# Kernel optimization log

Hardware: AMD Instinct MI355X
Metric: run time of the kernel (lower is better)

Reference implementation:

```python
import jax, jax.numpy as jnp
import numpy as np

K_NEIGHBOURS = 16


def setup_inputs() -> dict:
    key = jax.random.key(0)
    k1, k2 = jax.random.split(key)
    receivers = jax.random.normal(k1, (8, 2048, 128), dtype=jnp.float32)
    senders = jax.random.normal(k2, (8, 2048, 128), dtype=jnp.float32)
    return {"receivers": receivers, "senders": senders}


def reference(receivers, senders):
    B, Ns, Fs = senders.shape
    Nr = receivers.shape[1]
    k = K_NEIGHBOURS

    # pairwise squared euclidean distances [B, Ns, Nr]
    mixed = -2.0 * jnp.einsum('bsf,brf->bsr', senders, receivers)
    x2 = jnp.sum(senders * senders, axis=-1)[:, :, None]
    y2 = jnp.sum(receivers * receivers, axis=-1)[:, None, :]
    dist = jnp.abs(mixed + x2 + y2)

    # k nearest receivers per sender (no self_connection handling: default False)
    _, idx = jax.lax.top_k(-dist, k)  # [B, Ns, k]
    # tf.boolean_mask flattens in row-major order, so edges appear in
    # ascending receiver-index order within each sender row
    idx = jnp.sort(idx, axis=-1)

    # dense sender connectivity matrix (== sum of one-hots over k)
    b_ix = jnp.arange(B)[:, None, None]
    s_ix = jnp.arange(Ns)[None, :, None]
    sender = jnp.zeros((B, Ns, Nr), dtype=senders.dtype).at[b_ix, s_ix, idx].set(1.0)

    # gather edge endpoints; connectivity entries are exactly 1 so the
    # sender-matrix multiply + boolean_mask reduces to a plain gather
    sending = jnp.broadcast_to(senders[:, :, None, :], (B, Ns, k, Fs)).reshape(B * Ns * k, Fs)
    receiving = receivers[b_ix, idx].reshape(B * Ns * k, receivers.shape[-1])  # [B,Ns,k,Fr]

    edges = jnp.concatenate([sending, receiving], axis=-1)  # 'concat' aggregation
    return edges, sender
```

## Files before the change

kernel.cpp:

```cpp
#include <hip/hip_runtime.h>
#include <cstdint>

#define K_NE 16
constexpr int B = 8, N = 2048, F = 128;
constexpr size_t NSEND = (size_t)B * N;
constexpr size_t EDGE_FLOATS = NSEND * K_NE * 256;
constexpr size_t SEND_FLOATS = (size_t)B * N * N;

typedef _Float16 half8 __attribute__((ext_vector_type(8)));
typedef _Float16 half2v __attribute__((ext_vector_type(2)));
typedef float floatx4 __attribute__((ext_vector_type(4)));

#define SCALE 2048.0f
#define INV_SC2 2.384185791015625e-07f
#define F16_MIN_NORM 6.103515625e-05f

__global__ __launch_bounds__(256) void prep_kernel(const float* __restrict__ S,
                                                   const float* __restrict__ Rv,
                                                   float* __restrict__ x2,
                                                   float* __restrict__ y2,
                                                   _Float16* __restrict__ SH,
                                                   _Float16* __restrict__ SL,
                                                   _Float16* __restrict__ RH,
                                                   _Float16* __restrict__ RL) {
    const int tid = blockIdx.x * 256 + threadIdx.x;
    const int w = tid >> 6, lane = tid & 63;
    const bool isR = w >= (int)NSEND;
    const int row = isR ? w - (int)NSEND : w;
    const float* X = isR ? Rv : S;
    _Float16* H = isR ? RH : SH;
    _Float16* L = isR ? RL : SL;
    float* nrm = isR ? y2 : x2;

    const float2 v = ((const float2*)(X + (size_t)row * F))[lane];
    float s = v.x * v.x + v.y * v.y;
    #pragma unroll
    for (int off = 32; off; off >>= 1) s += __shfl_xor(s, off);
    if (lane == 0) nrm[row] = s;

    const float a0 = v.x * SCALE, a1 = v.y * SCALE;
    _Float16 h0 = (_Float16)a0;
    if (fabsf((float)h0) < F16_MIN_NORM) h0 = (_Float16)0.0f;
    _Float16 l0 = (_Float16)(a0 - (float)h0);
    if (fabsf((float)l0) < F16_MIN_NORM) l0 = (_Float16)0.0f;
    _Float16 h1 = (_Float16)a1;
    if (fabsf((float)h1) < F16_MIN_NORM) h1 = (_Float16)0.0f;
    _Float16 l1 = (_Float16)(a1 - (float)h1);
    if (fabsf((float)l1) < F16_MIN_NORM) l1 = (_Float16)0.0f;
    half2v hv = {h0, h1}, lv = {l0, l1};
    *(half2v*)(H + (size_t)row * F + lane * 2) = hv;
    *(half2v*)(L + (size_t)row * F + lane * 2) = lv;
}

__global__ __launch_bounds__(512) void score_mfma_kernel(
        const _Float16* __restrict__ SH, const _Float16* __restrict__ SL,
        const _Float16* __restrict__ RH, const _Float16* __restrict__ RL,
        const float* __restrict__ x2, const float* __restrict__ y2,
        float* __restrict__ scores) {
    __shared__ __attribute__((aligned(16))) _Float16 lA[2][2][4][128][8];
    __shared__ __attribute__((aligned(16))) _Float16 lB[2][2][4][128][8];
    const int bx = blockIdx.x, by = blockIdx.y, bz = blockIdx.z;
    const int t = threadIdx.x, lane = t & 63, wv = t >> 6;
    const int wrow0 = (wv >> 2) * 64;
    const int wcol0 = (wv & 3) * 32;
    const int lr = lane & 15, kg = lane >> 4;

    int s_h[2], s_kg[2], s_row[2];
    #pragma unroll
    for (int i = 0; i < 2; ++i) {
        const int s = t + (i << 9);
        s_h[i]   = s >> 9;
        s_row[i] = (s & 511) >> 2;
        s_kg[i]  = s & 3;
    }
    const size_t baseA = (size_t)(bz * N + by * 128);
    const size_t baseB = (size_t)(bz * N + bx * 128);

    #pragma unroll
    for (int i = 0; i < 2; ++i) {
        const _Float16* sa = (s_h[i] ? SL : SH) + (baseA + s_row[i]) * F + s_kg[i] * 8;
        const _Float16* sb = (s_h[i] ? RL : RH) + (baseB + s_row[i]) * F + s_kg[i] * 8;
        *(half8*)&lA[0][s_h[i]][s_kg[i]][s_row[i]][0] = *(const half8*)sa;
        *(half8*)&lB[0][s_h[i]][s_kg[i]][s_row[i]][0] = *(const half8*)sb;
    }
    __syncthreads();

    floatx4 acc[4][2] = {};

    #pragma unroll
    for (int kc = 0; kc < 4; ++kc) {
        const int cur = kc & 1;
        half8 pa[2], pb[2];
        if (kc < 3) {
            const int ko = (kc + 1) * 32;
            #pragma unroll
            for (int i = 0; i < 2; ++i) {
                pa[i] = *(const half8*)((s_h[i] ? SL : SH) + (baseA + s_row[i]) * F + ko + s_kg[i] * 8);
                pb[i] = *(const half8*)((s_h[i] ? RL : RH) + (baseB + s_row[i]) * F + ko + s_kg[i] * 8);
            }
        }
        half8 ah[4], al[4];
        #pragma unroll
        for (int i = 0; i < 4; ++i) {
            ah[i] = *(const half8*)&lA[cur][0][kg][wrow0 + i * 16 + lr][0];
            al[i] = *(const half8*)&lA[cur][1][kg][wrow0 + i * 16 + lr][0];
        }
        #pragma unroll
        for (int j = 0; j < 2; ++j) {
            const half8 bh = *(const half8*)&lB[cur][0][kg][wcol0 + j * 16 + lr][0];
            const half8 bl = *(const half8*)&lB[cur][1][kg][wcol0 + j * 16 + lr][0];
            #pragma unroll
            for (int i = 0; i < 4; ++i) {
                acc[i][j] = __builtin_amdgcn_mfma_f32_16x16x32_f16(ah[i], bh, acc[i][j], 0, 0, 0);
                acc[i][j] = __builtin_amdgcn_mfma_f32_16x16x32_f16(ah[i], bl, acc[i][j], 0, 0, 0);
                acc[i][j] = __builtin_amdgcn_mfma_f32_16x16x32_f16(al[i], bh, acc[i][j], 0, 0, 0);
            }
        }
        if (kc < 3) {
            const int nxt = cur ^ 1;
            #pragma unroll
            for (int i = 0; i < 2; ++i) {
                *(half8*)&lA[nxt][s_h[i]][s_kg[i]][s_row[i]][0] = pa[i];
                *(half8*)&lB[nxt][s_h[i]][s_kg[i]][s_row[i]][0] = pb[i];
            }
            __syncthreads();
        }
    }

    float* outb = scores + (size_t)bz * N * N;
    const float* x2b = x2 + (size_t)bz * N;
    const float* y2b = y2 + (size_t)bz * N;
    #pragma unroll
    for (int j = 0; j < 2; ++j) {
        const int col = bx * 128 + wcol0 + j * 16 + lr;
        const float yv = y2b[col];
        #pragma unroll
        for (int i = 0; i < 4; ++i) {
            #pragma unroll
            for (int r = 0; r < 4; ++r) {
                const int row = by * 128 + wrow0 + i * 16 + (lane >> 4) * 4 + r;
                const float d = acc[i][j][r] * INV_SC2;
                outb[(size_t)row * N + col] = fabsf((-2.0f * d + x2b[row]) + yv);
            }
        }
    }
}

#define KEYC(U, C) ((C) == 0 ? (U).x : (C) == 1 ? (U).y : (C) == 2 ? (U).z : (U).w)

__global__ __launch_bounds__(256) void topk_fused_kernel(const float* __restrict__ S,
                                                         const float* __restrict__ Rv,
                                                         float* __restrict__ scores,
                                                         float* __restrict__ edges_out) {
    __shared__ double candbuf[4][64];
    const int t = threadIdx.x;
    const int lane = t & 63;
    const int w = t >> 6;
    const int g = blockIdx.x * 4 + w;
    const int bz = g >> 11;
    double* cbuf = candbuf[w];
    float* srowp = scores + (size_t)g * N;
    const uint4* sr = (const uint4*)srowp;
    const double MAGIC = 4503599627370496.0;

    uint4 u[8];
    uint32_t mk = 0xFFFFFFFFu;
    #pragma unroll
    for (int jj = 0; jj < 8; ++jj) {
        u[jj] = sr[jj * 64 + lane];
        mk = mk < u[jj].x ? mk : u[jj].x;
        mk = mk < u[jj].y ? mk : u[jj].y;
        mk = mk < u[jj].z ? mk : u[jj].z;
        mk = mk < u[jj].w ? mk : u[jj].w;
    }

    uint32_t v = mk;
    #pragma unroll
    for (int k = 2; k <= 64; k <<= 1) {
        #pragma unroll
        for (int j = k >> 1; j >= 1; j >>= 1) {
            uint32_t o = (uint32_t)__shfl_xor((int)v, j);
            const bool take_min = (((lane & j) == 0) == ((lane & k) == 0));
            const uint32_t mn = v < o ? v : o;
            const uint32_t mx = v < o ? o : v;
            v = take_min ? mn : mx;
        }
    }
    const uint32_t T16 = (uint32_t)__shfl((int)v, 15);

    int myc = 0;
    #pragma unroll
    for (int jj = 0; jj < 8; ++jj)
        #pragma unroll
        for (int c = 0; c < 4; ++c)
            myc += (KEYC(u[jj], c) <= T16) ? 1 : 0;
    int off = myc;
    #pragma unroll
    for (int d = 1; d < 64; d <<= 1) {
        const int o = __shfl_up(off, d);
        if (lane >= d) off += o;
    }
    const int total = __shfl(off, 63);
    const int base = off - myc;

    int ixs[16];
    if (total <= 64) {
        int p = base;
        #pragma unroll
        for (int jj = 0; jj < 8; ++jj)
            #pragma unroll
            for (int c = 0; c < 4; ++c) {
                const uint32_t key = KEYC(u[jj], c);
                if (key <= T16) {
                    cbuf[p] = (double)key * 2048.0 + (double)(jj * 256 + lane * 4 + c);
                    ++p;
                }
            }
        double d = (lane < total) ? cbuf[lane] : 1e300;
        #pragma unroll
        for (int k = 2; k <= 64; k <<= 1) {
            #pragma unroll
            for (int j = k >> 1; j >= 1; j >>= 1) {
                const double o = __shfl_xor(d, j);
                const bool take_min = (((lane & j) == 0) == ((lane & k) == 0));
                d = take_min ? fmin(d, o) : fmax(d, o);
            }
        }
        const int myidx = (int)(__double_as_longlong(d + MAGIC) & 2047);
        #pragma unroll
        for (int e = 0; e < 16; ++e) ixs[e] = __shfl(myidx, e);
    } else {
        uint32_t fk = 0xFFFFFFFFu, fi = 0;
        #pragma unroll
        for (int jj = 0; jj < 8; ++jj) {
            const uint32_t bse = (uint32_t)(jj * 256 + lane * 4);
            if (u[jj].x < fk) { fk = u[jj].x; fi = bse; }
            if (u[jj].y < fk) { fk = u[jj].y; fi = bse + 1; }
            if (u[jj].z < fk) { fk = u[jj].z; fi = bse + 2; }
            if (u[jj].w < fk) { fk = u[jj].w; fi = bse + 3; }
        }
        #pragma unroll
        for (int it = 0; it < 16; ++it) {
            const uint32_t ck = fk, ci = fi;
            uint32_t gk = fk, gi = fi;
            #pragma unroll
            for (int o2 = 32; o2; o2 >>= 1) {
                uint32_t ok = (uint32_t)__shfl_xor((int)gk, o2);
                uint32_t oi = (uint32_t)__shfl_xor((int)gi, o2);
                if (ok < gk || (ok == gk && oi < gi)) { gk = ok; gi = oi; }
            }
            ixs[it] = (int)gi;
            if (ck == gk && ci == gi) {
                const int djj = (int)(gi >> 8), dc = (int)(gi & 3);
                #pragma unroll
                for (int jj = 0; jj < 8; ++jj)
                    if (jj == djj) {
                        if (dc == 0) u[jj].x = 0xFFFFFFFFu;
                        else if (dc == 1) u[jj].y = 0xFFFFFFFFu;
                        else if (dc == 2) u[jj].z = 0xFFFFFFFFu;
                        else u[jj].w = 0xFFFFFFFFu;
                    }
                fk = 0xFFFFFFFFu; fi = 0;
                #pragma unroll
                for (int jj = 0; jj < 8; ++jj) {
                    const uint32_t bse = (uint32_t)(jj * 256 + lane * 4);
                    if (u[jj].x < fk) { fk = u[jj].x; fi = bse; }
                    if (u[jj].y < fk) { fk = u[jj].y; fi = bse + 1; }
                    if (u[jj].z < fk) { fk = u[jj].z; fi = bse + 2; }
                    if (u[jj].w < fk) { fk = u[jj].w; fi = bse + 3; }
                }
            }
        }
    }

    int rank[16];
    #pragma unroll
    for (int e = 0; e < 16; ++e) {
        int r = 0;
        #pragma unroll
        for (int f = 0; f < 16; ++f) r += (ixs[f] < ixs[e]) ? 1 : 0;
        rank[e] = r;
    }

    uint32_t mask = 0;
    #pragma unroll
    for (int e = 0; e < 16; ++e) {
        const int ix = ixs[e];
        const int lane_t = (ix >> 2) & 63;
        const int bitpos = ((ix >> 8) << 2) | (ix & 3);
        if (lane == lane_t) mask |= (1u << bitpos);
    }
    #pragma unroll
    for (int j = 0; j < 8; ++j) {
        float4 vv;
        vv.x = (mask >> (j * 4 + 0)) & 1u ? 1.f : 0.f;
        vv.y = (mask >> (j * 4 + 1)) & 1u ? 1.f : 0.f;
        vv.z = (mask >> (j * 4 + 2)) & 1u ? 1.f : 0.f;
        vv.w = (mask >> (j * 4 + 3)) & 1u ? 1.f : 0.f;
        *(float4*)(srowp + j * 256 + lane * 4) = vv;
    }

    const float* srow = S + (size_t)g * F;
    const float* rb = Rv + (size_t)bz * N * F;
    float4 vs = {0.f, 0.f, 0.f, 0.f};
    if (lane < 32) vs = *(const float4*)(srow + lane * 4);
    #pragma unroll
    for (int e = 0; e < 16; ++e) {
        float4 vv = vs;
        if (lane >= 32)
            vv = *(const float4*)(rb + (size_t)ixs[e] * F + (lane - 32) * 4);
        *(float4*)(edges_out + ((size_t)g * K_NE + rank[e]) * 256 + lane * 4) = vv;
    }
}

extern "C" void kernel_launch(void* const* d_in, const int* in_sizes, int n_in,
                              void* d_out, int out_size, void* d_ws, size_t ws_size,
                              hipStream_t stream) {
    (void)in_sizes; (void)n_in; (void)out_size; (void)ws_size;
    const float* recv = (const float*)d_in[0];
    const float* send = (const float*)d_in[1];
    float* out = (float*)d_out;
    float* sender_mat = out + EDGE_FLOATS;
    float* x2 = (float*)((char*)d_ws + (262144u * 4));
    float* y2 = x2 + NSEND;

    _Float16* SH = (_Float16*)out;
    _Float16* SL = SH + NSEND * F;
    _Float16* RH = SL + NSEND * F;
    _Float16* RL = RH + NSEND * F;

    prep_kernel<<<8192, 256, 0, stream>>>(send, recv, x2, y2, SH, SL, RH, RL);
    dim3 g1(16, 16, 8);
    score_mfma_kernel<<<g1, 512, 0, stream>>>(SH, SL, RH, RL, x2, y2, sender_mat);
    topk_fused_kernel<<<4096, 256, 0, stream>>>(send, recv, sender_mat, out);
}
```

Baseline: 157.1 us.

## Fuse score MFMA and top-k into one kernel with scores held in LDS

The separate f16 hi/lo prep, tiled score GEMM and top-k kernels are replaced by one fused kernel. Each 1024-thread block takes 16 senders, computes their distances to all 2048 receivers with MFMA, keeps them in a 128KB LDS buffer, and runs top-k from there. This removes the full B×N×N score write and read-back through global memory. In exchange every block re-reads and re-converts all receivers from fp32, so receiver data reuse drops to 16 rows per block, and the large LDS footprint allows only one block per CU.

```diff
diff --git a/kernel.cpp b/kernel.cpp
--- a/kernel.cpp
+++ b/kernel.cpp
@@ -5,169 +5,119 @@
 constexpr int B = 8, N = 2048, F = 128;
 constexpr size_t NSEND = (size_t)B * N;
 constexpr size_t EDGE_FLOATS = NSEND * K_NE * 256;
-constexpr size_t SEND_FLOATS = (size_t)B * N * N;
+constexpr int SPB = 16;
 
 typedef _Float16 half8 __attribute__((ext_vector_type(8)));
-typedef _Float16 half2v __attribute__((ext_vector_type(2)));
 typedef float floatx4 __attribute__((ext_vector_type(4)));
 
 #define SCALE 2048.0f
 #define INV_SC2 2.384185791015625e-07f
 #define F16_MIN_NORM 6.103515625e-05f
 
-__global__ __launch_bounds__(256) void prep_kernel(const float* __restrict__ S,
-                                                   const float* __restrict__ Rv,
-                                                   float* __restrict__ x2,
-                                                   float* __restrict__ y2,
-                                                   _Float16* __restrict__ SH,
-                                                   _Float16* __restrict__ SL,
-                                                   _Float16* __restrict__ RH,
-                                                   _Float16* __restrict__ RL) {
-    const int tid = blockIdx.x * 256 + threadIdx.x;
-    const int w = tid >> 6, lane = tid & 63;
-    const bool isR = w >= (int)NSEND;
-    const int row = isR ? w - (int)NSEND : w;
-    const float* X = isR ? Rv : S;
-    _Float16* H = isR ? RH : SH;
-    _Float16* L = isR ? RL : SL;
-    float* nrm = isR ? y2 : x2;
-
-    const float2 v = ((const float2*)(X + (size_t)row * F))[lane];
+__global__ __launch_bounds__(256) void norms_kernel(const float* __restrict__ X,
+                                                    float* __restrict__ out) {
+    int tid = blockIdx.x * 256 + threadIdx.x;
+    int w = tid >> 6, lane = tid & 63;
+    const float2 v = ((const float2*)(X + (size_t)w * F))[lane];
     float s = v.x * v.x + v.y * v.y;
     #pragma unroll
     for (int off = 32; off; off >>= 1) s += __shfl_xor(s, off);
-    if (lane == 0) nrm[row] = s;
-
-    const float a0 = v.x * SCALE, a1 = v.y * SCALE;
-    _Float16 h0 = (_Float16)a0;
-    if (fabsf((float)h0) < F16_MIN_NORM) h0 = (_Float16)0.0f;
-    _Float16 l0 = (_Float16)(a0 - (float)h0);
-    if (fabsf((float)l0) < F16_MIN_NORM) l0 = (_Float16)0.0f;
-    _Float16 h1 = (_Float16)a1;
-    if (fabsf((float)h1) < F16_MIN_NORM) h1 = (_Float16)0.0f;
-    _Float16 l1 = (_Float16)(a1 - (float)h1);
-    if (fabsf((float)l1) < F16_MIN_NORM) l1 = (_Float16)0.0f;
-    half2v hv = {h0, h1}, lv = {l0, l1};
-    *(half2v*)(H + (size_t)row * F + lane * 2) = hv;
-    *(half2v*)(L + (size_t)row * F + lane * 2) = lv;
-}
-
-__global__ __launch_bounds__(512) void score_mfma_kernel(
-        const _Float16* __restrict__ SH, const _Float16* __restrict__ SL,
-        const _Float16* __restrict__ RH, const _Float16* __restrict__ RL,
-        const float* __restrict__ x2, const float* __restrict__ y2,
-        float* __restrict__ scores) {
-    __shared__ __attribute__((aligned(16))) _Float16 lA[2][2][4][128][8];
-    __shared__ __attribute__((aligned(16))) _Float16 lB[2][2][4][128][8];
-    const int bx = blockIdx.x, by = blockIdx.y, bz = blockIdx.z;
+    if (lane == 0) out[w] = s;
+}
+
+__device__ __forceinline__ void cvt_hilo(float a, _Float16& h, _Float16& l) {
+    a *= SCALE;
+    h = (_Float16)a;
+    if (fabsf((float)h) < F16_MIN_NORM) h = (_Float16)0.0f;
+    l = (_Float16)(a - (float)h);
+    if (fabsf((float)l) < F16_MIN_NORM) l = (_Float16)0.0f;
+}
+
+#define KEYC(U, C) ((C) == 0 ? (U).x : (C) == 1 ? (U).y : (C) == 2 ? (U).z : (U).w)
+
+__global__ __launch_bounds__(1024) void fused_kernel(const float* __restrict__ S,
+                                                     const float* __restrict__ Rv,
+                                                     const float* __restrict__ x2,
+                                                     const float* __restrict__ y2,
+                                                     float* __restrict__ conn,
+                                                     float* __restrict__ edges_out) {
+    __shared__ uint32_t keys[SPB][N];
+    __shared__ double candbuf[16][64];
     const int t = threadIdx.x, lane = t & 63, wv = t >> 6;
-    const int wrow0 = (wv >> 2) * 64;
-    const int wcol0 = (wv & 3) * 32;
-    const int lr = lane & 15, kg = lane >> 4;
-
-    int s_h[2], s_kg[2], s_row[2];
-    #pragma unroll
-    for (int i = 0; i < 2; ++i) {
-        const int s = t + (i << 9);
-        s_h[i]   = s >> 9;
-        s_row[i] = (s & 511) >> 2;
-        s_kg[i]  = s & 3;
-    }
-    const size_t baseA = (size_t)(bz * N + by * 128);
-    const size_t baseB = (size_t)(bz * N + bx * 128);
-
-    #pragma unroll
-    for (int i = 0; i < 2; ++i) {
-        const _Float16* sa = (s_h[i] ? SL : SH) + (baseA + s_row[i]) * F + s_kg[i] * 8;
-        const _Float16* sb = (s_h[i] ? RL : RH) + (baseB + s_row[i]) * F + s_kg[i] * 8;
-        *(half8*)&lA[0][s_h[i]][s_kg[i]][s_row[i]][0] = *(const half8*)sa;
-        *(half8*)&lB[0][s_h[i]][s_kg[i]][s_row[i]][0] = *(const half8*)sb;
+    const int blk = blockIdx.x;
+    const int bz = blk >> 7;
+    const int sg0 = (blk & 127) * SPB;
+    const int lr = lane & 15, kgrp = lane >> 4;
+    const double MAGIC = 4503599627370496.0;
+
+    const float* x2b = x2 + bz * N;
+    const float* y2b = y2 + bz * N;
+    const float* rbase = Rv + (size_t)bz * N * F;
+
+    half8 ah[4], al[4];
+    {
+        const float* arow = S + ((size_t)(bz * N + sg0) + lr) * F;
+        #pragma unroll
+        for (int ks = 0; ks < 4; ++ks) {
+            const int k0 = ks * 32 + kgrp * 8;
+            const float4 f0 = *(const float4*)(arow + k0);
+            const float4 f1 = *(const float4*)(arow + k0 + 4);
+            const float av[8] = {f0.x, f0.y, f0.z, f0.w, f1.x, f1.y, f1.z, f1.w};
+            #pragma unroll
+            for (int j = 0; j < 8; ++j) {
+                _Float16 hh, ll;
+                cvt_hilo(av[j], hh, ll);
+                ah[ks][j] = hh;
+                al[ks][j] = ll;
+            }
+        }
+    }
+    float xr[4];
+    #pragma unroll
+    for (int r = 0; r < 4; ++r) xr[r] = x2b[sg0 + kgrp * 4 + r];
+
+    #pragma unroll 1
+    for (int ct = 0; ct < 8; ++ct) {
+        const int col0 = wv * 128 + ct * 16;
+        const float* brow = rbase + (size_t)(col0 + lr) * F;
+        floatx4 acc = {0.f, 0.f, 0.f, 0.f};
+        #pragma unroll
+        for (int ks = 0; ks < 4; ++ks) {
+            const int k0 = ks * 32 + kgrp * 8;
+            const float4 f0 = *(const float4*)(brow + k0);
+            const float4 f1 = *(const float4*)(brow + k0 + 4);
+            const float bv[8] = {f0.x, f0.y, f0.z, f0.w, f1.x, f1.y, f1.z, f1.w};
+            half8 bh, bl;
+            #pragma unroll
+            for (int j = 0; j < 8; ++j) {
+                _Float16 hh, ll;
+                cvt_hilo(bv[j], hh, ll);
+                bh[j] = hh;
+                bl[j] = ll;
+            }
+            acc = __builtin_amdgcn_mfma_f32_16x16x32_f16(ah[ks], bh, acc, 0, 0, 0);
+            acc = __builtin_amdgcn_mfma_f32_16x16x32_f16(ah[ks], bl, acc, 0, 0, 0);
+            acc = __builtin_amdgcn_mfma_f32_16x16x32_f16(al[ks], bh, acc, 0, 0, 0);
+        }
+        const float yv = y2b[col0 + lr];
+        #pragma unroll
+        for (int r = 0; r < 4; ++r) {
+            const float d = acc[r] * INV_SC2;
+            const float sc = fabsf((-2.0f * d + xr[r]) + yv);
+            keys[kgrp * 4 + r][col0 + lr] = __float_as_uint(sc);
+        }
     }
     __syncthreads();
 
-    floatx4 acc[4][2] = {};
-
-    #pragma unroll
-    for (int kc = 0; kc < 4; ++kc) {
-        const int cur = kc & 1;
-        half8 pa[2], pb[2];
-        if (kc < 3) {
-            const int ko = (kc + 1) * 32;
-            #pragma unroll
-            for (int i = 0; i < 2; ++i) {
-                pa[i] = *(const half8*)((s_h[i] ? SL : SH) + (baseA + s_row[i]) * F + ko + s_kg[i] * 8);
-                pb[i] = *(const half8*)((s_h[i] ? RL : RH) + (baseB + s_row[i]) * F + ko + s_kg[i] * 8);
-            }
-        }
-        half8 ah[4], al[4];
-        #pragma unroll
-        for (int i = 0; i < 4; ++i) {
-            ah[i] = *(const half8*)&lA[cur][0][kg][wrow0 + i * 16 + lr][0];
-            al[i] = *(const half8*)&lA[cur][1][kg][wrow0 + i * 16 + lr][0];
-        }
-        #pragma unroll
-        for (int j = 0; j < 2; ++j) {
-            const half8 bh = *(const half8*)&lB[cur][0][kg][wcol0 + j * 16 + lr][0];
-            const half8 bl = *(const half8*)&lB[cur][1][kg][wcol0 + j * 16 + lr][0];
-            #pragma unroll
-            for (int i = 0; i < 4; ++i) {
-                acc[i][j] = __builtin_amdgcn_mfma_f32_16x16x32_f16(ah[i], bh, acc[i][j], 0, 0, 0);
-                acc[i][j] = __builtin_amdgcn_mfma_f32_16x16x32_f16(ah[i], bl, acc[i][j], 0, 0, 0);
-                acc[i][j] = __builtin_amdgcn_mfma_f32_16x16x32_f16(al[i], bh, acc[i][j], 0, 0, 0);
-            }
-        }
-        if (kc < 3) {
-            const int nxt = cur ^ 1;
-            #pragma unroll
-            for (int i = 0; i < 2; ++i) {
-                *(half8*)&lA[nxt][s_h[i]][s_kg[i]][s_row[i]][0] = pa[i];
-                *(half8*)&lB[nxt][s_h[i]][s_kg[i]][s_row[i]][0] = pb[i];
-            }
-            __syncthreads();
-        }
-    }
-
-    float* outb = scores + (size_t)bz * N * N;
-    const float* x2b = x2 + (size_t)bz * N;
-    const float* y2b = y2 + (size_t)bz * N;
-    #pragma unroll
-    for (int j = 0; j < 2; ++j) {
-        const int col = bx * 128 + wcol0 + j * 16 + lr;
-        const float yv = y2b[col];
-        #pragma unroll
-        for (int i = 0; i < 4; ++i) {
-            #pragma unroll
-            for (int r = 0; r < 4; ++r) {
-                const int row = by * 128 + wrow0 + i * 16 + (lane >> 4) * 4 + r;
-                const float d = acc[i][j][r] * INV_SC2;
-                outb[(size_t)row * N + col] = fabsf((-2.0f * d + x2b[row]) + yv);
-            }
-        }
-    }
-}
-
-#define KEYC(U, C) ((C) == 0 ? (U).x : (C) == 1 ? (U).y : (C) == 2 ? (U).z : (U).w)
-
-__global__ __launch_bounds__(256) void topk_fused_kernel(const float* __restrict__ S,
-                                                         const float* __restrict__ Rv,
-                                                         float* __restrict__ scores,
-                                                         float* __restrict__ edges_out) {
-    __shared__ double candbuf[4][64];
-    const int t = threadIdx.x;
-    const int lane = t & 63;
-    const int w = t >> 6;
-    const int g = blockIdx.x * 4 + w;
-    const int bz = g >> 11;
-    double* cbuf = candbuf[w];
-    float* srowp = scores + (size_t)g * N;
-    const uint4* sr = (const uint4*)srowp;
-    const double MAGIC = 4503599627370496.0;
+    const int g = bz * N + sg0 + wv;
+    double* cbuf = candbuf[wv];
+    const uint4* krow = (const uint4*)keys[wv];
 
     uint4 u[8];
     uint32_t mk = 0xFFFFFFFFu;
     #pragma unroll
     for (int jj = 0; jj < 8; ++jj) {
-        u[jj] = sr[jj * 64 + lane];
+        u[jj] = krow[jj * 64 + lane];
         mk = mk < u[jj].x ? mk : u[jj].x;
         mk = mk < u[jj].y ? mk : u[jj].y;
         mk = mk < u[jj].z ? mk : u[jj].z;
@@ -290,6 +240,7 @@
         const int bitpos = ((ix >> 8) << 2) | (ix & 3);
         if (lane == lane_t) mask |= (1u << bitpos);
     }
+    float* crow = conn + (size_t)g * N;
     #pragma unroll
     for (int j = 0; j < 8; ++j) {
         float4 vv;
@@ -297,18 +248,17 @@
         vv.y = (mask >> (j * 4 + 1)) & 1u ? 1.f : 0.f;
         vv.z = (mask >> (j * 4 + 2)) & 1u ? 1.f : 0.f;
         vv.w = (mask >> (j * 4 + 3)) & 1u ? 1.f : 0.f;
-        *(float4*)(srowp + j * 256 + lane * 4) = vv;
+        *(float4*)(crow + j * 256 + lane * 4) = vv;
     }
 
     const float* srow = S + (size_t)g * F;
-    const float* rb = Rv + (size_t)bz * N * F;
     float4 vs = {0.f, 0.f, 0.f, 0.f};
     if (lane < 32) vs = *(const float4*)(srow + lane * 4);
     #pragma unroll
     for (int e = 0; e < 16; ++e) {
         float4 vv = vs;
         if (lane >= 32)
-            vv = *(const float4*)(rb + (size_t)ixs[e] * F + (lane - 32) * 4);
+            vv = *(const float4*)(rbase + (size_t)ixs[e] * F + (lane - 32) * 4);
         *(float4*)(edges_out + ((size_t)g * K_NE + rank[e]) * 256 + lane * 4) = vv;
     }
 }
@@ -320,17 +270,11 @@
     const float* recv = (const float*)d_in[0];
     const float* send = (const float*)d_in[1];
     float* out = (float*)d_out;
-    float* sender_mat = out + EDGE_FLOATS;
+    float* conn = out + EDGE_FLOATS;
     float* x2 = (float*)((char*)d_ws + (262144u * 4));
     float* y2 = x2 + NSEND;
 
-    _Float16* SH = (_Float16*)out;
-    _Float16* SL = SH + NSEND * F;
-    _Float16* RH = SL + NSEND * F;
-    _Float16* RL = RH + NSEND * F;
-
-    prep_kernel<<<8192, 256, 0, stream>>>(send, recv, x2, y2, SH, SL, RH, RL);
-    dim3 g1(16, 16, 8);
-    score_mfma_kernel<<<g1, 512, 0, stream>>>(SH, SL, RH, RL, x2, y2, sender_mat);
-    topk_fused_kernel<<<4096, 256, 0, stream>>>(send, recv, sender_mat, out);
-}
+    norms_kernel<<<4096, 256, 0, stream>>>(send, x2);
+    norms_kernel<<<4096, 256, 0, stream>>>(recv, y2);
+    fused_kernel<<<1024, 1024, 0, stream>>>(send, recv, x2, y2, conn, out);
+}
```

Result: slower. 222.1 us (+41.3%).
